# Kernel optimization log

Measured on AMD Instinct MI355X. Metric: run time of the kernel, lower is better.

Reference implementation:

```python
import jax, jax.numpy as jnp
import numpy as np

ALPHA = 1.702
LIMIT = 7.0

# Tiling: A*B*M = BD*S (total dispatched tokens)
A, B, E, M, H, I = 2, 8, 16, 128, 2048, 2048
_BD, _S = 2, 1024


def setup_inputs() -> dict:
    key = jax.random.key(0)
    ks = jax.random.split(key, 6)
    inv_h = 1.0 / np.sqrt(H)
    inv_i = 1.0 / np.sqrt(I)
    return {
        "dispatched": jax.random.normal(ks[0], (A, B, E, M, H), dtype=jnp.float32),
        "gate_up_proj": jax.random.normal(ks[1], (E, H, 2 * I), dtype=jnp.float32) * inv_h,
        "gate_up_proj_bias": jax.random.normal(ks[2], (E, 2 * I), dtype=jnp.float32) * 0.02,
        "down_proj": jax.random.normal(ks[3], (E, I, H), dtype=jnp.float32) * inv_i,
        "down_proj_bias": jax.random.normal(ks[4], (E, H), dtype=jnp.float32) * 0.02,
        "sparsity_remap": jax.random.randint(ks[5], (E, E), 0, E, dtype=jnp.int32),
        "BD": _BD,
        "S": _S,
    }


def _moe_activation_gpt_oss(gate_up_out):
    # interleaved gate/up: [g0,u0,g1,u1,...]
    gate = gate_up_out[..., ::2]
    up = gate_up_out[..., 1::2]
    gate = jnp.minimum(gate, LIMIT)
    up = jnp.clip(up, -LIMIT, LIMIT)
    glu = gate * jax.nn.sigmoid(gate * ALPHA)
    return (up + 1.0) * glu


def reference(dispatched, gate_up_proj, gate_up_proj_bias, down_proj,
              down_proj_bias, sparsity_remap, BD, S):
    # sparsity_remap is an opaque tile remap for tt.sparse_matmul; the dense
    # grouped matmul computes the same math (zero tiles contribute zeros).
    a, b, e, m, h = dispatched.shape
    inter = gate_up_proj.shape[-1] // 2
    # grouped gate_up GEMM: [A,B,E,M,H] @ [E,H,2I] -> [A,B,E,M,2I]
    gate_up_out = jnp.einsum('abemh,ehn->abemn', dispatched, gate_up_proj)
    gate_up_out = gate_up_out + gate_up_proj_bias[None, None, :, None, :]
    activated = _moe_activation_gpt_oss(gate_up_out)  # [A,B,E,M,I]
    activated = activated.reshape(a * b, e, m, inter)
    # grouped down GEMM: [AB,E,M,I] @ [E,I,H] -> [AB,E,M,H]
    down_out = jnp.einsum('xemi,eih->xemh', activated, down_proj)
    down_out = down_out + down_proj_bias[None, :, None, :]
    # untile: [AB,E,M,H] -> [AB,M,E,H] -> [BD,S,E,H]
    down_out = jnp.transpose(down_out, (0, 2, 1, 3))
    return down_out.reshape(BD, S, e, h)
```

## Files before the change

### kernel.cpp

```cpp
#include <hip/hip_runtime.h>
#include <stdint.h>

#define DEV __device__ __forceinline__

constexpr int E_ = 16, M_ = 128, H_ = 2048, I_ = 2048;
constexpr int X_ = 16;
constexpr int N1 = 2 * I_;
constexpr int ROWS = X_ * M_;

typedef short bfrag __attribute__((ext_vector_type(8)));
typedef float ffrag __attribute__((ext_vector_type(4)));
typedef unsigned short us8 __attribute__((ext_vector_type(8)));

DEV unsigned short f2bf(float f) {
    union { float f; unsigned u; } v; v.f = f;
    unsigned u = v.u;
    u += 0x7fffu + ((u >> 16) & 1u);
    return (unsigned short)(u >> 16);
}

DEV void gload16(const void* g, void* lds_wave_base) {
    __builtin_amdgcn_global_load_lds(
        (const __attribute__((address_space(1))) unsigned int*)g,
        (__attribute__((address_space(3))) unsigned int*)lds_wave_base,
        16, 0, 0);
}

DEV void block_bar() {
    asm volatile("" ::: "memory");
    __builtin_amdgcn_s_barrier();
    asm volatile("" ::: "memory");
}


__global__ __launch_bounds__(256) void convert_a(const float* __restrict__ in,
                                                 unsigned short* __restrict__ outb) {
    const int n4 = X_ * E_ * M_ * H_ / 4;
    int idx = blockIdx.x * 256 + threadIdx.x;
    int stride = gridDim.x * 256;
    for (int f = idx; f < n4; f += stride) {
        float4 v = ((const float4*)in)[f];
        ushort4 o;
        o.x = f2bf(v.x); o.y = f2bf(v.y); o.z = f2bf(v.z); o.w = f2bf(v.w);
        const int c = f & 511;
        const int row = f >> 9;
        const int m = row & 127, e = (row >> 7) & 15, x = row >> 11;
        ((ushort4*)outb)[((size_t)(e * ROWS + x * M_ + m) << 9) + c] = o;
    }
}

__global__ __launch_bounds__(256) void convert_b1(const float* __restrict__ gup,
                                                  unsigned short* __restrict__ b1t) {
    const int e = blockIdx.x, h0 = blockIdx.y * 64, n0 = blockIdx.z * 128;
    __shared__ float tile[64][129];
    const float* src = gup + (size_t)e * H_ * N1;
    const int t = threadIdx.x;
#pragma unroll
    for (int i = 0; i < 8; ++i) {
        int idx = i * 1024 + t * 4;
        int r = idx >> 7, c = idx & 127;
        float4 v = *(const float4*)(src + (size_t)(h0 + r) * N1 + n0 + c);
        tile[r][c] = v.x; tile[r][c + 1] = v.y; tile[r][c + 2] = v.z; tile[r][c + 3] = v.w;
    }
    __syncthreads();
    const int p = t >> 2;
    const int hh = (t & 3) * 16;
    us8 g0, g1, u0, u1;
#pragma unroll
    for (int k = 0; k < 8; ++k) {
        g0[k] = f2bf(tile[hh + k][2 * p]);
        u0[k] = f2bf(tile[hh + k][2 * p + 1]);
        g1[k] = f2bf(tile[hh + 8 + k][2 * p]);
        u1[k] = f2bf(tile[hh + 8 + k][2 * p + 1]);
    }
    unsigned short* dg = b1t + ((size_t)e * N1 + (n0 >> 1) + p) * H_ + h0 + hh;
    unsigned short* du = b1t + ((size_t)e * N1 + I_ + (n0 >> 1) + p) * H_ + h0 + hh;
    *(us8*)dg = g0; *(us8*)(dg + 8) = g1;
    *(us8*)du = u0; *(us8*)(du + 8) = u1;
}

__global__ __launch_bounds__(256) void convert_b2(const float* __restrict__ dwn,
                                                  unsigned short* __restrict__ b2t) {
    const int e = blockIdx.x, i0 = blockIdx.y * 64, h0 = blockIdx.z * 64;
    __shared__ float tile[64][65];
    const float* src = dwn + (size_t)e * I_ * H_;
    const int t = threadIdx.x;
#pragma unroll
    for (int it = 0; it < 4; ++it) {
        int idx = it * 1024 + t * 4;
        int r = idx >> 6, c = idx & 63;
        float4 v = *(const float4*)(src + (size_t)(i0 + r) * H_ + h0 + c);
        tile[r][c] = v.x; tile[r][c + 1] = v.y; tile[r][c + 2] = v.z; tile[r][c + 3] = v.w;
    }
    __syncthreads();
    const int hl = t >> 2, ii = (t & 3) * 16;
    us8 o0, o1;
#pragma unroll
    for (int k = 0; k < 8; ++k) {
        o0[k] = f2bf(tile[ii + k][hl]);
        o1[k] = f2bf(tile[ii + 8 + k][hl]);
    }
    unsigned short* d = b2t + ((size_t)e * H_ + h0 + hl) * I_ + i0 + ii;
    *(us8*)d = o0; *(us8*)(d + 8) = o1;
}

template <int MODE>
__global__ __launch_bounds__(512, 2) void gemm8p(
    const unsigned short* __restrict__ A,
    const unsigned short* __restrict__ B,
    const float* __restrict__ bias,
    void* __restrict__ outv)
{
    constexpr int LD = 2048;
    constexpr int NT = 2048 / 64;

    __shared__ unsigned short lds[2][2][256 * 64];

    const int t = threadIdx.x, wave = t >> 6, lane = t & 63;
    const int wr = wave >> 2, wc = wave & 3;

    int id = blockIdx.x;
    const int cpx = gridDim.x >> 3;
    id = (id & 7) * cpx + (id >> 3);
    int e, mt, bt;
    if (MODE == 0) { e = id >> 7; mt = (id >> 4) & 7; bt = id & 15; }
    else           { e = id >> 6; mt = (id >> 3) & 7; bt = id & 7; }

    const unsigned short* Aexp = A + ((size_t)e * ROWS + mt * 256) * LD;
    const unsigned short* Bexp = (MODE == 0)
        ? B + (size_t)e * N1 * LD
        : B + ((size_t)e * H_ + bt * 256) * LD;

    ffrag acc[8][4];
#pragma unroll
    for (int i = 0; i < 8; ++i)
#pragma unroll
        for (int j = 0; j < 4; ++j) acc[i][j] = ffrag{0.f, 0.f, 0.f, 0.f};

    const int rsub = lane >> 3;
    const int csw = ((lane & 7) ^ (lane >> 3)) * 8;

    auto stage = [&](int kt, int b) {
        const int k0 = kt * 64;
#pragma unroll
        for (int i = 0; i < 4; ++i) {
            const int Rb = (wave * 4 + i) * 8;
            const int r = Rb + rsub;
            gload16(Aexp + (size_t)r * LD + k0 + csw, (void*)&lds[b][0][Rb * 64]);
        }
#pragma unroll
        for (int i = 0; i < 4; ++i) {
            const int Rb = (wave * 4 + i) * 8;
            const int r = Rb + rsub;
            int grow;
            if (MODE == 0)
                grow = ((r >> 5) & 1) * I_ + bt * 128 + (r >> 6) * 32 + (r & 31);
            else
                grow = r;
            gload16(Bexp + (size_t)grow * LD + k0 + csw, (void*)&lds[b][1][Rb * 64]);
        }
    };

    stage(0, 0);

    const int l15 = lane & 15, lr16 = lane >> 4, sw = lane & 7;
    const int arow0 = wr * 128 + l15;
    const int brow0 = wc * 64 + l15;

#pragma unroll 2
    for (int kt = 0; kt < NT; ++kt) {
        const int cur = kt & 1;
        if (kt + 1 < NT) {
            stage(kt + 1, cur ^ 1);
            __builtin_amdgcn_sched_barrier(0);
            asm volatile("s_waitcnt vmcnt(8)" ::: "memory");
        } else {
            asm volatile("s_waitcnt vmcnt(0)" ::: "memory");
        }
        __builtin_amdgcn_sched_barrier(0);
        block_bar();

        bfrag bAll[4][2];
        bfrag af[4][2];

#pragma unroll
        for (int nf = 0; nf < 4; ++nf)
#pragma unroll
            for (int ks = 0; ks < 2; ++ks)
                bAll[nf][ks] = *(const bfrag*)&lds[cur][1][(brow0 + nf * 16) * 64 + (((ks * 4 + lr16) ^ sw) * 8)];
#pragma unroll
        for (int mf = 0; mf < 4; ++mf)
#pragma unroll
            for (int ks = 0; ks < 2; ++ks)
                af[mf][ks] = *(const bfrag*)&lds[cur][0][(arow0 + mf * 16) * 64 + (((ks * 4 + lr16) ^ sw) * 8)];
        block_bar();
        asm volatile("s_waitcnt lgkmcnt(0)" ::: "memory");
        __builtin_amdgcn_sched_barrier(0);
        __builtin_amdgcn_s_setprio(1);
#pragma unroll
        for (int mf = 0; mf < 4; ++mf)
#pragma unroll
            for (int nf = 0; nf < 4; ++nf)
#pragma unroll
                for (int ks = 0; ks < 2; ++ks)
                    acc[mf][nf] = __builtin_amdgcn_mfma_f32_16x16x32_bf16(
                        af[mf][ks], bAll[nf][ks], acc[mf][nf], 0, 0, 0);
        __builtin_amdgcn_s_setprio(0);
        block_bar();

#pragma unroll
        for (int mf = 0; mf < 4; ++mf)
#pragma unroll
            for (int ks = 0; ks < 2; ++ks)
                af[mf][ks] = *(const bfrag*)&lds[cur][0][(arow0 + 64 + mf * 16) * 64 + (((ks * 4 + lr16) ^ sw) * 8)];
        block_bar();
        asm volatile("s_waitcnt lgkmcnt(0)" ::: "memory");
        __builtin_amdgcn_sched_barrier(0);
        __builtin_amdgcn_s_setprio(1);
#pragma unroll
        for (int mf = 0; mf < 4; ++mf)
#pragma unroll
            for (int nf = 0; nf < 4; ++nf)
#pragma unroll
                for (int ks = 0; ks < 2; ++ks)
                    acc[4 + mf][nf] = __builtin_amdgcn_mfma_f32_16x16x32_bf16(
                        af[mf][ks], bAll[nf][ks], acc[4 + mf][nf], 0, 0, 0);
        __builtin_amdgcn_s_setprio(0);
        block_bar();
    }

    const int rb = mt * 256 + wr * 128 + lr16 * 4;
    if (MODE == 0) {
        unsigned short* act = (unsigned short*)outv + (size_t)e * ROWS * I_;
#pragma unroll
        for (int nf = 0; nf < 2; ++nf) {
            const int jj = bt * 128 + wc * 32 + nf * 16 + l15;
            const float gb = bias[(size_t)e * N1 + 2 * jj];
            const float ub = bias[(size_t)e * N1 + 2 * jj + 1];
#pragma unroll
            for (int mf = 0; mf < 8; ++mf)
#pragma unroll
                for (int r = 0; r < 4; ++r) {
                    float g = acc[mf][nf][r] + gb;
                    float u = acc[mf][2 + nf][r] + ub;
                    g = fminf(g, 7.0f);
                    u = fminf(fmaxf(u, -7.0f), 7.0f);
                    const float glu = g / (1.0f + __expf(-1.702f * g));
                    const float av = (u + 1.0f) * glu;
                    act[(size_t)(rb + mf * 16 + r) * I_ + jj] = f2bf(av);
                }
        }
    } else {
        float* out = (float*)outv;
#pragma unroll
        for (int nf = 0; nf < 4; ++nf) {
            const int h = bt * 256 + wc * 64 + nf * 16 + l15;
            const float bb = bias[(size_t)e * H_ + h];
#pragma unroll
            for (int mf = 0; mf < 8; ++mf)
#pragma unroll
                for (int r = 0; r < 4; ++r) {
                    const int row = rb + mf * 16 + r;
                    out[((size_t)row * E_ + e) * H_ + h] = acc[mf][nf][r] + bb;
                }
        }
    }
}


extern "C" void kernel_launch(void* const* d_in, const int* in_sizes, int n_in,
                              void* d_out, int out_size, void* d_ws, size_t ws_size,
                              hipStream_t stream) {
    const float* disp  = (const float*)d_in[0];
    const float* gup   = (const float*)d_in[1];
    const float* gub   = (const float*)d_in[2];
    const float* down  = (const float*)d_in[3];
    const float* dbias = (const float*)d_in[4];
    float* out = (float*)d_out;

    const size_t NEED = (size_t)512 << 20;
    if (ws_size < NEED) {
        hipMemsetAsync(d_out, 0, (size_t)out_size * sizeof(float), stream);
        return;
    }
    unsigned short* a_bf = (unsigned short*)d_ws;
    unsigned short* b1t  = (unsigned short*)((char*)d_ws + ((size_t)128 << 20));
    unsigned short* b2t  = b1t;
    unsigned short* actb = (unsigned short*)((char*)d_ws + ((size_t)384 << 20));

    convert_a<<<4096, 256, 0, stream>>>(disp, a_bf);
    convert_b1<<<dim3(E_, H_ / 64, N1 / 128), 256, 0, stream>>>(gup, b1t);
    gemm8p<0><<<2048, 512, 0, stream>>>(a_bf, b1t, gub, actb);
    convert_b2<<<dim3(E_, I_ / 64, H_ / 64), 256, 0, stream>>>(down, b2t);
    gemm8p<1><<<1024, 512, 0, stream>>>(actb, b2t, dbias, out);
}
```

Baseline: 1.237 ms.

## Split B-fragment loads into halves and interleave four MFMA phases per k-tile

```diff
diff --git a/kernel.cpp b/kernel.cpp
--- a/kernel.cpp
+++ b/kernel.cpp
@@ -180,19 +180,20 @@
         __builtin_amdgcn_sched_barrier(0);
         block_bar();
 
-        bfrag bAll[4][2];
+        bfrag bB0[2][2], bB1[2][2];
         bfrag af[4][2];
 
 #pragma unroll
-        for (int nf = 0; nf < 4; ++nf)
+        for (int nf = 0; nf < 2; ++nf)
 #pragma unroll
             for (int ks = 0; ks < 2; ++ks)
-                bAll[nf][ks] = *(const bfrag*)&lds[cur][1][(brow0 + nf * 16) * 64 + (((ks * 4 + lr16) ^ sw) * 8)];
+                bB0[nf][ks] = *(const bfrag*)&lds[cur][1][(brow0 + nf * 16) * 64 + (((ks * 4 + lr16) ^ sw) * 8)];
 #pragma unroll
         for (int mf = 0; mf < 4; ++mf)
 #pragma unroll
             for (int ks = 0; ks < 2; ++ks)
                 af[mf][ks] = *(const bfrag*)&lds[cur][0][(arow0 + mf * 16) * 64 + (((ks * 4 + lr16) ^ sw) * 8)];
+        asm volatile("s_waitcnt lgkmcnt(8)" ::: "memory");
         block_bar();
         asm volatile("s_waitcnt lgkmcnt(0)" ::: "memory");
         __builtin_amdgcn_sched_barrier(0);
@@ -200,19 +201,19 @@
 #pragma unroll
         for (int mf = 0; mf < 4; ++mf)
 #pragma unroll
-            for (int nf = 0; nf < 4; ++nf)
+            for (int nf = 0; nf < 2; ++nf)
 #pragma unroll
                 for (int ks = 0; ks < 2; ++ks)
                     acc[mf][nf] = __builtin_amdgcn_mfma_f32_16x16x32_bf16(
-                        af[mf][ks], bAll[nf][ks], acc[mf][nf], 0, 0, 0);
+                        af[mf][ks], bB0[nf][ks], acc[mf][nf], 0, 0, 0);
         __builtin_amdgcn_s_setprio(0);
         block_bar();
 
 #pragma unroll
-        for (int mf = 0; mf < 4; ++mf)
+        for (int nf = 0; nf < 2; ++nf)
 #pragma unroll
             for (int ks = 0; ks < 2; ++ks)
-                af[mf][ks] = *(const bfrag*)&lds[cur][0][(arow0 + 64 + mf * 16) * 64 + (((ks * 4 + lr16) ^ sw) * 8)];
+                bB1[nf][ks] = *(const bfrag*)&lds[cur][1][(brow0 + 32 + nf * 16) * 64 + (((ks * 4 + lr16) ^ sw) * 8)];
         block_bar();
         asm volatile("s_waitcnt lgkmcnt(0)" ::: "memory");
         __builtin_amdgcn_sched_barrier(0);
@@ -220,11 +221,44 @@
 #pragma unroll
         for (int mf = 0; mf < 4; ++mf)
 #pragma unroll
-            for (int nf = 0; nf < 4; ++nf)
+            for (int nf = 0; nf < 2; ++nf)
+#pragma unroll
+                for (int ks = 0; ks < 2; ++ks)
+                    acc[mf][2 + nf] = __builtin_amdgcn_mfma_f32_16x16x32_bf16(
+                        af[mf][ks], bB1[nf][ks], acc[mf][2 + nf], 0, 0, 0);
+        __builtin_amdgcn_s_setprio(0);
+        block_bar();
+
+#pragma unroll
+        for (int mf = 0; mf < 4; ++mf)
+#pragma unroll
+            for (int ks = 0; ks < 2; ++ks)
+                af[mf][ks] = *(const bfrag*)&lds[cur][0][(arow0 + 64 + mf * 16) * 64 + (((ks * 4 + lr16) ^ sw) * 8)];
+        block_bar();
+        asm volatile("s_waitcnt lgkmcnt(0)" ::: "memory");
+        __builtin_amdgcn_sched_barrier(0);
+        __builtin_amdgcn_s_setprio(1);
+#pragma unroll
+        for (int mf = 0; mf < 4; ++mf)
+#pragma unroll
+            for (int nf = 0; nf < 2; ++nf)
+#pragma unroll
+                for (int ks = 0; ks < 2; ++ks)
+                    acc[4 + mf][2 + nf] = __builtin_amdgcn_mfma_f32_16x16x32_bf16(
+                        af[mf][ks], bB1[nf][ks], acc[4 + mf][2 + nf], 0, 0, 0);
+        __builtin_amdgcn_s_setprio(0);
+        block_bar();
+
+        block_bar();
+        __builtin_amdgcn_s_setprio(1);
+#pragma unroll
+        for (int mf = 0; mf < 4; ++mf)
+#pragma unroll
+            for (int nf = 0; nf < 2; ++nf)
 #pragma unroll
                 for (int ks = 0; ks < 2; ++ks)
                     acc[4 + mf][nf] = __builtin_amdgcn_mfma_f32_16x16x32_bf16(
-                        af[mf][ks], bAll[nf][ks], acc[4 + mf][nf], 0, 0, 0);
+                        af[mf][ks], bB0[nf][ks], acc[4 + mf][nf], 0, 0, 0);
         __builtin_amdgcn_s_setprio(0);
         block_bar();
     }
```

New measurement: 1.242 ms. About the same (+0.4%).

## Switch GEMM mainloop to BK=32 with four-stage LDS ring and deeper prefetch

Applied to the files above, without the earlier changes.

```diff
diff --git a/kernel.cpp b/kernel.cpp
--- a/kernel.cpp
+++ b/kernel.cpp
@@ -112,9 +112,10 @@
     void* __restrict__ outv)
 {
     constexpr int LD = 2048;
-    constexpr int NT = 2048 / 64;
-
-    __shared__ unsigned short lds[2][2][256 * 64];
+    constexpr int BK = 32;
+    constexpr int NT = 2048 / BK;
+
+    __shared__ unsigned short lds[4][2][256 * BK];
 
     const int t = threadIdx.x, wave = t >> 6, lane = t & 63;
     const int wr = wave >> 2, wc = wave & 3;
@@ -137,96 +138,86 @@
 #pragma unroll
         for (int j = 0; j < 4; ++j) acc[i][j] = ffrag{0.f, 0.f, 0.f, 0.f};
 
-    const int rsub = lane >> 3;
-    const int csw = ((lane & 7) ^ (lane >> 3)) * 8;
+    const int rsub = lane >> 2;
+    const int csw = ((lane & 3) ^ ((lane >> 3) & 3)) * 8;
 
     auto stage = [&](int kt, int b) {
-        const int k0 = kt * 64;
-#pragma unroll
-        for (int i = 0; i < 4; ++i) {
-            const int Rb = (wave * 4 + i) * 8;
+        const int k0 = kt * BK;
+#pragma unroll
+        for (int i = 0; i < 2; ++i) {
+            const int Rb = (wave * 2 + i) * 16;
             const int r = Rb + rsub;
-            gload16(Aexp + (size_t)r * LD + k0 + csw, (void*)&lds[b][0][Rb * 64]);
-        }
-#pragma unroll
-        for (int i = 0; i < 4; ++i) {
-            const int Rb = (wave * 4 + i) * 8;
+            gload16(Aexp + (size_t)r * LD + k0 + csw, (void*)&lds[b][0][Rb * BK]);
+        }
+#pragma unroll
+        for (int i = 0; i < 2; ++i) {
+            const int Rb = (wave * 2 + i) * 16;
             const int r = Rb + rsub;
             int grow;
             if (MODE == 0)
                 grow = ((r >> 5) & 1) * I_ + bt * 128 + (r >> 6) * 32 + (r & 31);
             else
                 grow = r;
-            gload16(Bexp + (size_t)grow * LD + k0 + csw, (void*)&lds[b][1][Rb * 64]);
+            gload16(Bexp + (size_t)grow * LD + k0 + csw, (void*)&lds[b][1][Rb * BK]);
         }
     };
 
     stage(0, 0);
-
-    const int l15 = lane & 15, lr16 = lane >> 4, sw = lane & 7;
+    stage(1, 1);
+    stage(2, 2);
+
+    const int l15 = lane & 15, lr16 = lane >> 4;
+    const int swl = (l15 >> 1) & 3;
+    const int kch = (lr16 ^ swl) * 8;
     const int arow0 = wr * 128 + l15;
     const int brow0 = wc * 64 + l15;
 
-#pragma unroll 2
+#pragma unroll 4
     for (int kt = 0; kt < NT; ++kt) {
-        const int cur = kt & 1;
-        if (kt + 1 < NT) {
-            stage(kt + 1, cur ^ 1);
-            __builtin_amdgcn_sched_barrier(0);
-            asm volatile("s_waitcnt vmcnt(8)" ::: "memory");
-        } else {
-            asm volatile("s_waitcnt vmcnt(0)" ::: "memory");
-        }
+        const int cur = kt & 3;
+
+        if (kt + 2 < NT)      { asm volatile("s_waitcnt vmcnt(8)" ::: "memory"); }
+        else if (kt + 1 < NT) { asm volatile("s_waitcnt vmcnt(4)" ::: "memory"); }
+        else                  { asm volatile("s_waitcnt vmcnt(0)" ::: "memory"); }
         __builtin_amdgcn_sched_barrier(0);
         block_bar();
 
-        bfrag bAll[4][2];
-        bfrag af[4][2];
+        bfrag bB[4], af[8];
 
 #pragma unroll
         for (int nf = 0; nf < 4; ++nf)
-#pragma unroll
-            for (int ks = 0; ks < 2; ++ks)
-                bAll[nf][ks] = *(const bfrag*)&lds[cur][1][(brow0 + nf * 16) * 64 + (((ks * 4 + lr16) ^ sw) * 8)];
+            bB[nf] = *(const bfrag*)&lds[cur][1][(brow0 + nf * 16) * BK + kch];
 #pragma unroll
         for (int mf = 0; mf < 4; ++mf)
-#pragma unroll
-            for (int ks = 0; ks < 2; ++ks)
-                af[mf][ks] = *(const bfrag*)&lds[cur][0][(arow0 + mf * 16) * 64 + (((ks * 4 + lr16) ^ sw) * 8)];
-        block_bar();
+            af[mf] = *(const bfrag*)&lds[cur][0][(arow0 + mf * 16) * BK + kch];
+        asm volatile("" ::: "memory");
+#pragma unroll
+        for (int mf = 4; mf < 8; ++mf)
+            af[mf] = *(const bfrag*)&lds[cur][0][(arow0 + mf * 16) * BK + kch];
+
+        if (kt + 3 < NT) stage(kt + 3, (kt + 3) & 3);
+
+        asm volatile("s_waitcnt lgkmcnt(4)" ::: "memory");
+        __builtin_amdgcn_sched_barrier(0);
+        __builtin_amdgcn_s_setprio(1);
+#pragma unroll
+        for (int mf = 0; mf < 4; ++mf)
+#pragma unroll
+            for (int nf = 0; nf < 4; ++nf)
+                acc[mf][nf] = __builtin_amdgcn_mfma_f32_16x16x32_bf16(
+                    af[mf], bB[nf], acc[mf][nf], 0, 0, 0);
+        __builtin_amdgcn_s_setprio(0);
+
         asm volatile("s_waitcnt lgkmcnt(0)" ::: "memory");
         __builtin_amdgcn_sched_barrier(0);
         __builtin_amdgcn_s_setprio(1);
 #pragma unroll
-        for (int mf = 0; mf < 4; ++mf)
+        for (int mf = 4; mf < 8; ++mf)
 #pragma unroll
             for (int nf = 0; nf < 4; ++nf)
-#pragma unroll
-                for (int ks = 0; ks < 2; ++ks)
-                    acc[mf][nf] = __builtin_amdgcn_mfma_f32_16x16x32_bf16(
-                        af[mf][ks], bAll[nf][ks], acc[mf][nf], 0, 0, 0);
+                acc[mf][nf] = __builtin_amdgcn_mfma_f32_16x16x32_bf16(
+                    af[mf], bB[nf], acc[mf][nf], 0, 0, 0);
         __builtin_amdgcn_s_setprio(0);
-        block_bar();
-
-#pragma unroll
-        for (int mf = 0; mf < 4; ++mf)
-#pragma unroll
-            for (int ks = 0; ks < 2; ++ks)
-                af[mf][ks] = *(const bfrag*)&lds[cur][0][(arow0 + 64 + mf * 16) * 64 + (((ks * 4 + lr16) ^ sw) * 8)];
-        block_bar();
-        asm volatile("s_waitcnt lgkmcnt(0)" ::: "memory");
-        __builtin_amdgcn_sched_barrier(0);
-        __builtin_amdgcn_s_setprio(1);
-#pragma unroll
-        for (int mf = 0; mf < 4; ++mf)
-#pragma unroll
-            for (int nf = 0; nf < 4; ++nf)
-#pragma unroll
-                for (int ks = 0; ks < 2; ++ks)
-                    acc[4 + mf][nf] = __builtin_amdgcn_mfma_f32_16x16x32_bf16(
-                        af[mf][ks], bAll[nf][ks], acc[4 + mf][nf], 0, 0, 0);
-        __builtin_amdgcn_s_setprio(0);
-        block_bar();
     }
 
     const int rb = mt * 256 + wr * 128 + lr16 * 4;
```

Measured after the change: 1.185 ms. -4.2%, faster.
